# Kernel optimization log

Hardware: AMD Instinct MI355X
Metric: run time of the kernel (lower is better)

The kernel has to match this reference:

```python
import jax, jax.numpy as jnp
import numpy as np

N, P = 25000, 400000          # atoms, pairs
F, E, EH = 64, 32, 64         # nr_atom_basis, nr_edge_basis, nr_edge_basis_hidden
FH, SSH, S = 64, 64, 64       # node hidden, spatial hidden, spatial
FV, C, H, K = 64, 32, 4, 50   # velocity hidden, coefficients, heads, rbf
R_MAX = 0.5                   # maximum_interaction_radius (nm)
EPS = 1e-8
SCALE = 1.0                   # scale_factor_in_nanometer


def physnet_rbf(d):
    # PhysNet RBF: exp(-beta * (exp(-d) - mu_k)^2), mu_k in [exp(-r_max), 1]
    mu = jnp.linspace(np.exp(-R_MAX), 1.0, K).astype(jnp.float32)
    beta = jnp.float32(((2.0 / K) * (1.0 - np.exp(-R_MAX))) ** -2)
    return jnp.exp(-beta * (jnp.exp(-d)[:, None] - mu) ** 2)  # [P, K]


def seg_sum(v, idx, n):
    return jax.ops.segment_sum(v, idx, num_segments=n)


def seg_mean(v, idx, n):
    # matches torch scatter_reduce 'mean' with include_self=False (empty segments -> 0)
    s = seg_sum(v, idx, n)
    cnt = seg_sum(jnp.ones((v.shape[0],), v.dtype), idx, n)
    cnt = jnp.maximum(cnt, 1.0).reshape((n,) + (1,) * (v.ndim - 1))
    return s / cnt


def seg_softmax(a, idx, n):
    # numerically-stable per-receiver softmax over variable neighbor sets
    m = jax.ops.segment_max(a, idx, num_segments=n)
    m = jnp.where(jnp.isfinite(m), m, 0.0)
    e = jnp.exp(a - m[idx])
    return e / seg_sum(e, idx, n)[idx]


def setup_inputs():
    key = jax.random.key(0)
    ks = jax.random.split(key, 20)
    def w(k, shape):
        return jax.random.normal(k, shape, jnp.float32) * 0.05
    z = lambda *s: jnp.zeros(s, jnp.float32)
    return dict(
        h=jax.random.normal(ks[0], (N, F), jnp.float32),
        x=jax.random.uniform(ks[1], (N, 3), jnp.float32),
        v=jax.random.normal(ks[2], (N, 3), jnp.float32) * 0.1,
        idx_i=jax.random.randint(ks[3], (P,), 0, N),
        idx_j=jax.random.randint(ks[4], (P,), 0, N),
        W_ein=w(ks[5], (2 * F, K)), b_ein=z(K),
        W_eo1=w(ks[6], (2 * F + K + 1, EH)), b_eo1=z(EH),
        W_eo2=w(ks[7], (EH, E)), b_eo2=z(E),
        W_att=w(ks[8], (E, H)), b_att=z(H),
        W_xm=w(ks[9], (H * E, C)),
        W_vm=w(ks[10], (C,)),
        W_pn1=w(ks[11], (C, SSH)), b_pn1=z(SSH),
        W_pn2=w(ks[12], (SSH, S)), b_pn2=z(S),
        W_n1=w(ks[13], (F + H * E + S, FH)), b_n1=z(FH),
        W_n2=w(ks[14], (FH, F)), b_n2=z(F),
        W_v1=w(ks[15], (F, FV)), b_v1=z(FV),
        W_v2=w(ks[16], (FV, 1)),
    )


def reference(h, x, v, idx_i, idx_j,
              W_ein, b_ein, W_eo1, b_eo1, W_eo2, b_eo2,
              W_att, b_att, W_xm, W_vm,
              W_pn1, b_pn1, W_pn2, b_pn2,
              W_n1, b_n1, W_n2, b_n2,
              W_v1, b_v1, W_v2):
    act = jax.nn.silu
    # geometry
    r_ij = x[idx_j] - x[idx_i]                       # [P, 3]
    d_ij = jnp.sqrt(jnp.sum(r_ij ** 2, axis=-1) + EPS)
    dir_ij = r_ij / (d_ij[:, None] + EPS)
    # edge update (Eq. 7): RBF-filtered edge MLP
    h_cat = jnp.concatenate([h[idx_i], h[idx_j]], axis=-1)          # [P, 2F]
    filtered = physnet_rbf(d_ij) * (h_cat @ W_ein + b_ein)          # [P, K]
    edge_in = jnp.concatenate([h_cat, filtered, (d_ij / SCALE)[:, None]], axis=-1)
    h_ij_edge = act(edge_in @ W_eo1 + b_eo1) @ W_eo2 + b_eo2        # [P, E]
    # multi-head semantic attention: segment softmax per receiver
    att = jax.nn.celu(h_ij_edge @ W_att + b_att, alpha=2.0)         # [P, H]
    att_w = seg_softmax(att, idx_i, N)                              # [P, H]
    h_ij_sem = (h_ij_edge[:, :, None] * att_w[:, None, :]).reshape(P, E * H)
    # neighborhood aggregation
    h_i_sem = seg_sum(h_ij_sem, idx_i, N)                           # [N, E*H]
    # spatial attention (Eq. 6)
    comb = jnp.tanh(h_ij_sem @ W_xm)[:, :, None] * dir_ij[:, None, :]  # [P, C, 3]
    comb_mean = seg_mean(comb, idx_i, N)                            # [N, C, 3]
    comb_norm2 = jnp.sum(comb_mean ** 2, axis=-1)                   # [N, C]
    h_i_spatial = act(act(comb_norm2 @ W_pn1 + b_pn1) @ W_pn2 + b_pn2)
    # node update (Eq. 4)
    node_in = jnp.concatenate([h, h_i_sem, h_i_spatial], axis=-1)
    h_new = h + act(act(node_in @ W_n1 + b_n1) @ W_n2 + b_n2)
    # velocity update (Eq. 12)
    v_ij = jnp.einsum('pcx,c->px', comb, W_vm)                      # [P, 3]
    dv = seg_mean(v_ij, idx_i, N)                                   # [N, 3]
    gate = 2.0 * jax.nn.sigmoid(act(h_new @ W_v1 + b_v1) @ W_v2)    # [N, 1]
    v_new = gate * v + dv
    x_new = x + v_new
    return h_new, x_new, v_new
```

## Files before the change

kernel.cpp:

```cpp
#include <hip/hip_runtime.h>
#include <hip/hip_bf16.h>

#define DEV __device__ __forceinline__

constexpr int N_ = 25000;
constexpr int P_ = 400000;

constexpr int align4(int xx){ return (xx+3)&~3; }
constexpr int OFF_CNT     = 0;
constexpr int OFF_OFFSETS = align4(OFF_CNT + N_);
constexpr int OFF_CURSOR  = align4(OFF_OFFSETS + N_ + 1);
constexpr int OFF_EDGE    = align4(OFF_CURSOR + N_);
constexpr int OFF_E4      = OFF_EDGE + P_*16;
constexpr int OFF_DIR     = OFF_E4 + P_*4;
constexpr int OFF_SEM     = align4(OFF_DIR + P_*4);
constexpr int OFF_N2      = OFF_SEM + N_*64;
constexpr int OFF_DV      = OFF_N2 + N_*16;
constexpr int OFF_WB5     = OFF_DV + N_*4;
constexpr int OFF_WB6     = OFF_WB5 + 1024;
constexpr int OFF_WB7     = OFF_WB6 + 2048;
constexpr int OFF_WB8     = OFF_WB7 + 8192;
constexpr int OFF_WB9     = OFF_WB8 + 2048;
constexpr int OFF_HB      = OFF_WB9 + 2048;
constexpr int OFF_SIJ     = OFF_HB + N_*32;
constexpr int OFF_WB1     = OFF_SIJ + P_*2;
constexpr int OFF_WB2     = OFF_WB1 + 8192;
constexpr int OFF_WB3     = OFF_WB2 + 2048;
constexpr int OFF_WB4     = OFF_WB3 + 1024;
constexpr int WS_UNITS    = OFF_WB4 + 2048;

constexpr float MU0F  = 0.60653065971263342f;
constexpr float DMUF  = (1.0f - 0.60653065971263342f) / 49.0f;
constexpr float BETAF = 1.0f / ((0.04f * (1.0f - 0.60653065971263342f)) *
                                (0.04f * (1.0f - 0.60653065971263342f)));
constexpr float EPSF  = 1e-8f;

DEV float u2f(unsigned int u){ union{unsigned int i; float f;} c; c.i=u; return c.f; }
DEV unsigned int f2b16(float f){
  __hip_bfloat16 b = __float2bfloat16(f);
  unsigned short s; __builtin_memcpy(&s, &b, 2);
  return (unsigned int)s;
}
DEV unsigned int pack2(float a, float b){ return f2b16(a) | (f2b16(b) << 16); }
DEV float frcp(float x){ return __builtin_amdgcn_rcpf(x); }
DEV float silu_f(float v){ return v * frcp(1.0f + __expf(-v)); }

using short8 = __attribute__((ext_vector_type(8))) short;
using f32x4  = __attribute__((ext_vector_type(4))) float;
union U4S8 { uint4 u; short8 s; };
DEV short8 ld_frag(const void* p){ U4S8 c; c.u = *(const uint4*)p; return c.s; }
DEV f32x4 mfma16(short8 a, short8 b, f32x4 c){
  return __builtin_amdgcn_mfma_f32_16x16x32_bf16(a, b, c, 0, 0, 0);
}

__global__ void k_prep0(const int* __restrict__ idx_i,
                        const float* __restrict__ h,
                        const float* __restrict__ Wein, const float* __restrict__ Weo1,
                        const float* __restrict__ Weo2, const float* __restrict__ Wxm,
                        const float* __restrict__ Wpn1, const float* __restrict__ Wpn2,
                        const float* __restrict__ Wn1,  const float* __restrict__ Wn2,
                        const float* __restrict__ Wv1,
                        int* __restrict__ cnt, unsigned int* __restrict__ hb,
                        unsigned short* __restrict__ wb1, unsigned short* __restrict__ wb2,
                        unsigned short* __restrict__ wb3, unsigned short* __restrict__ wb4,
                        unsigned short* __restrict__ wb5, unsigned short* __restrict__ wb6,
                        unsigned short* __restrict__ wb7, unsigned short* __restrict__ wb8,
                        unsigned short* __restrict__ wb9){
  int t = blockIdx.x*256 + threadIdx.x;
  const int st = gridDim.x*256;
  if (t < P_) atomicAdd(&cnt[idx_i[t]], 1);
  for (int q=t; q<N_*32; q+=st){
    float2 a = *(const float2*)(h + (size_t)q*2);
    hb[q] = pack2(a.x, a.y);
  }
  for (int q=t; q<8*4*64*8; q+=st){
    int e=q&7, lane=(q>>3)&63, sx=(q>>9)&3, nf=q>>11;
    int l15=lane&15, quad=lane>>4;
    int n = 16*nf + l15, k = sx*32 + quad*8 + e;
    float v = (n<50) ? Wein[k*50+n] : ((n<64) ? 0.f : Weo1[k*64+(n-64)]);
    wb1[q] = (unsigned short)f2b16(v);
  }
  for (int q=t; q<4*2*64*8; q+=st){
    int e=q&7, lane=(q>>3)&63, sx=(q>>9)&1, nf=q>>10;
    int l15=lane&15, quad=lane>>4;
    int n = 16*nf + l15, k = sx*32 + quad*8 + e;
    float v = (k<50) ? Weo1[(128+k)*64+n] : ((k==50) ? Weo1[178*64+n] : 0.f);
    wb2[q] = (unsigned short)f2b16(v);
  }
  for (int q=t; q<2*2*64*8; q+=st){
    int e=q&7, lane=(q>>3)&63, sx=(q>>9)&1, nf=q>>10;
    int l15=lane&15, quad=lane>>4;
    int n = 16*nf + l15, k = sx*32 + quad*8 + e;
    wb3[q] = (unsigned short)f2b16(Weo2[k*32+n]);
  }
  for (int q=t; q<8*64*8; q+=st){
    int e=q&7, lane=(q>>3)&63, nf=q>>9;
    int l15=lane&15, quad=lane>>4;
    int k = quad*8 + e;
    int n_log = l15*8 + nf;
    int cc = n_log>>2, hh = n_log&3;
    wb4[q] = (unsigned short)f2b16(Wxm[(k*4+hh)*32 + cc]);
  }
  for (int q=t; q<4*64*8; q+=st){
    int e=q&7, lane=(q>>3)&63, nf=q>>9;
    int l15=lane&15, quad=lane>>4;
    int n = 16*nf + l15, k = quad*8 + e;
    wb5[q] = (unsigned short)f2b16(Wpn1[k*64+n]);
  }
  for (int q=t; q<4*2*64*8; q+=st){
    int e=q&7, lane=(q>>3)&63, sx=(q>>9)&1, nf=q>>10;
    int l15=lane&15, quad=lane>>4;
    int n = 16*nf + l15, k = sx*32 + quad*8 + e;
    wb6[q] = (unsigned short)f2b16(Wpn2[k*64+n]);
    wb8[q] = (unsigned short)f2b16(Wn2[k*64+n]);
    wb9[q] = (unsigned short)f2b16(Wv1[k*64+n]);
  }
  for (int q=t; q<4*8*64*8; q+=st){
    int e=q&7, lane=(q>>3)&63, sx=(q>>9)&7, nf=q>>12;
    int l15=lane&15, quad=lane>>4;
    int n = 16*nf + l15, k = sx*32 + quad*8 + e;
    wb7[q] = (unsigned short)f2b16(Wn1[k*64+n]);
  }
}

__global__ __launch_bounds__(1024) void k_scan(const int* __restrict__ cnt,
                                               int* __restrict__ offsets,
                                               int* __restrict__ cursor){
  __shared__ unsigned short sCnt[N_];
  __shared__ int swv[16];
  const int t = threadIdx.x;
  const int wv = t >> 6, ln = t & 63;
  for (int q = t; q < N_; q += 1024) sCnt[q] = (unsigned short)cnt[q];
  __syncthreads();
  constexpr int CH = (N_ + 1023)/1024;
  int b = t*CH, e = b+CH;
  if (b > N_) b = N_;
  if (e > N_) e = N_;
  int s = 0;
  for (int q=b; q<e; q++) s += sCnt[q];
  int incl = s;
  #pragma unroll
  for (int off=1; off<64; off<<=1){
    int vv = __shfl_up(incl, off);
    if (ln >= off) incl += vv;
  }
  if (ln == 63) swv[wv] = incl;
  __syncthreads();
  if (wv == 0 && ln < 16){
    int w = swv[ln];
    #pragma unroll
    for (int off=1; off<16; off<<=1){
      int vv = __shfl_up(w, off);
      if (ln >= off) w += vv;
    }
    swv[ln] = w;
  }
  __syncthreads();
  const int wpre = (wv > 0) ? swv[wv-1] : 0;
  int run = wpre + incl - s;
  for (int q=b; q<e; q++){
    int c0 = sCnt[q];
    offsets[q] = run; cursor[q] = run; run += c0;
  }
  if (t == 1023) offsets[N_] = run;
}

__global__ void k_scatter2(const int* __restrict__ idx_i, const int* __restrict__ idx_j,
                           int* __restrict__ cursor,
                           int* __restrict__ sij){
  int t = blockIdx.x*256 + threadIdx.x;
  if (t >= P_) return;
  int i = idx_i[t], j = idx_j[t];
  int pos = atomicAdd(&cursor[i], 1);
  *(int2*)(sij + (size_t)pos*2) = make_int2(i, j);
}

__global__ __launch_bounds__(256, 4) void k_edge2(
    const unsigned short* __restrict__ hb,
    const int* __restrict__ sij, const float* __restrict__ x,
    float* __restrict__ dir4,
    const unsigned short* __restrict__ wb1, const unsigned short* __restrict__ wb2,
    const unsigned short* __restrict__ wb3,
    const float* __restrict__ bein, const float* __restrict__ beo1,
    const float* __restrict__ beo2, const float* __restrict__ Watt,
    const float* __restrict__ batt,
    unsigned int* __restrict__ edge_out, float* __restrict__ e4_out)
{
  __shared__ __align__(16) unsigned char sAll[4*4608];
  __shared__ float sdv[128];
  __shared__ float semd[128];

  const int tid  = threadIdx.x;
  const int wv   = tid >> 6;
  const int lane = tid & 63;
  const int l15  = lane & 15;
  const int quad = lane >> 4;
  const int pbase = blockIdx.x * 128;
  unsigned char* sW = sAll + wv*4608;

  if (lane < 32){
    int row = 32*wv + lane;
    int2 ij = *(const int2*)(sij + (size_t)(pbase + row)*2);
    float xi0=x[ij.x*3], xi1=x[ij.x*3+1], xi2=x[ij.x*3+2];
    float xj0=x[ij.y*3], xj1=x[ij.y*3+1], xj2=x[ij.y*3+2];
    float rx=xj0-xi0, ry=xj1-xi1, rz=xj2-xi2;
    float d = sqrtf(rx*rx+ry*ry+rz*rz+EPSF);
    float iv = frcp(d+EPSF);
    sdv[row]  = d;
    semd[row] = __expf(-d);
    *(float4*)(dir4 + (size_t)(pbase + row)*4) = make_float4(rx*iv, ry*iv, rz*iv, d);
  }

  short8 af0[4], af1[4];
  {
    const int rbase = pbase + 32*wv;
    int2 ij0 = *(const int2*)(sij + (size_t)(rbase + l15)*2);
    int2 ij1 = *(const int2*)(sij + (size_t)(rbase + 16 + l15)*2);
    const unsigned char* hB = (const unsigned char*)hb;
    af0[0] = ld_frag(hB + (size_t)ij0.x*128 + quad*16);
    af0[1] = ld_frag(hB + (size_t)ij0.x*128 + 64 + quad*16);
    af0[2] = ld_frag(hB + (size_t)ij0.y*128 + quad*16);
    af0[3] = ld_frag(hB + (size_t)ij0.y*128 + 64 + quad*16);
    af1[0] = ld_frag(hB + (size_t)ij1.x*128 + quad*16);
    af1[1] = ld_frag(hB + (size_t)ij1.x*128 + 64 + quad*16);
    af1[2] = ld_frag(hB + (size_t)ij1.y*128 + quad*16);
    af1[3] = ld_frag(hB + (size_t)ij1.y*128 + 64 + quad*16);
  }

  f32x4 acc[2][4];
  #pragma unroll
  for (int mf=0; mf<2; mf++)
    #pragma unroll
    for (int nf=0; nf<4; nf++){
      int nn = 16*nf + l15;
      float bias = (nn < 50) ? bein[nn] : 0.f;
      acc[mf][nf] = (f32x4){bias, bias, bias, bias};
    }
  #pragma unroll
  for (int s=0; s<4; s++){
    #pragma unroll
    for (int nf=0; nf<4; nf++){
      short8 b = ld_frag((const unsigned char*)wb1 + (size_t)((nf*4 + s)*64 + lane)*16);
      acc[0][nf] = mfma16(af0[s], b, acc[0][nf]);
      acc[1][nf] = mfma16(af1[s], b, acc[1][nf]);
    }
  }

  #pragma unroll
  for (int mf=0; mf<2; mf++)
    #pragma unroll
    for (int nf=0; nf<4; nf++){
      int n = 16*nf + l15;
      float mu = MU0F + (float)n*DMUF;
      #pragma unroll
      for (int reg=0; reg<4; reg++){
        int lrow = 16*mf + quad*4 + reg;
        int grow = 32*wv + lrow;
        float t = semd[grow] - mu;
        float fv = acc[mf][nf][reg] * __expf(-BETAF*t*t);
        unsigned short ob;
        if (n < 50)       ob = (unsigned short)f2b16(fv);
        else if (n == 50) ob = (unsigned short)f2b16(sdv[grow]);
        else              ob = 0;
        ((unsigned short*)sW)[lrow*72 + n] = ob;
      }
    }

  #pragma unroll
  for (int mf=0; mf<2; mf++)
    #pragma unroll
    for (int nf=0; nf<4; nf++){
      float bias = beo1[16*nf + l15];
      acc[mf][nf] = (f32x4){bias, bias, bias, bias};
    }
  #pragma unroll
  for (int s=0; s<4; s++){
    #pragma unroll
    for (int nf=0; nf<4; nf++){
      short8 b = ld_frag((const unsigned char*)wb1 + (size_t)(((4+nf)*4 + s)*64 + lane)*16);
      acc[0][nf] = mfma16(af0[s], b, acc[0][nf]);
      acc[1][nf] = mfma16(af1[s], b, acc[1][nf]);
    }
  }

  #pragma unroll
  for (int s=0; s<2; s++){
    int koff = s*32 + quad*8;
    short8 a0 = ld_frag(sW + l15*144      + koff*2);
    short8 a1 = ld_frag(sW + (16+l15)*144 + koff*2);
    #pragma unroll
    for (int nf=0; nf<4; nf++){
      short8 b = ld_frag((const unsigned char*)wb2 + (size_t)((nf*2 + s)*64 + lane)*16);
      acc[0][nf] = mfma16(a0, b, acc[0][nf]);
      acc[1][nf] = mfma16(a1, b, acc[1][nf]);
    }
  }

  unsigned char* A3 = sW;
  #pragma unroll
  for (int mf=0; mf<2; mf++)
    #pragma unroll
    for (int nf=0; nf<4; nf++){
      int n = 16*nf + l15;
      #pragma unroll
      for (int reg=0; reg<4; reg++){
        int lrow = 16*mf + quad*4 + reg;
        ((unsigned short*)A3)[lrow*72 + n] = (unsigned short)f2b16(silu_f(acc[mf][nf][reg]));
      }
    }

  f32x4 acc3[2][2];
  #pragma unroll
  for (int mf=0; mf<2; mf++)
    #pragma unroll
    for (int nf=0; nf<2; nf++){
      float bias = beo2[16*nf + l15];
      acc3[mf][nf] = (f32x4){bias, bias, bias, bias};
    }
  #pragma unroll
  for (int s=0; s<2; s++){
    int koff = s*32 + quad*8;
    short8 a0 = ld_frag(A3 + l15*144      + koff*2);
    short8 a1 = ld_frag(A3 + (16+l15)*144 + koff*2);
    #pragma unroll
    for (int nf=0; nf<2; nf++){
      short8 b = ld_frag((const unsigned char*)wb3 + (size_t)((nf*2 + s)*64 + lane)*16);
      acc3[0][nf] = mfma16(a0, b, acc3[0][nf]);
      acc3[1][nf] = mfma16(a1, b, acc3[1][nf]);
    }
  }

  #pragma unroll
  for (int mf=0; mf<2; mf++)
    #pragma unroll
    for (int nf=0; nf<2; nf++){
      int n = 16*nf + l15;
      #pragma unroll
      for (int reg=0; reg<4; reg++){
        int lrow = 16*mf + quad*4 + reg;
        ((float*)sW)[lrow*36 + n] = acc3[mf][nf][reg];
      }
    }

  {
    int rr = lane >> 1;
    int p = pbase + 32*wv + rr;
    int cb = (lane & 1) * 16;
    const float* er = (const float*)(sW + rr*144);
    float l0, l1, l2, l3;
    if ((lane & 1) == 0){ l0 = batt[0]; l1 = batt[1]; l2 = batt[2]; l3 = batt[3]; }
    else                { l0 = l1 = l2 = l3 = 0.f; }
    float ecache[16];
    {
      float4 v0 = *(const float4*)(er + cb);
      float4 v1 = *(const float4*)(er + cb + 4);
      float4 v2 = *(const float4*)(er + cb + 8);
      float4 v3 = *(const float4*)(er + cb + 12);
      ecache[0]=v0.x; ecache[1]=v0.y; ecache[2]=v0.z; ecache[3]=v0.w;
      ecache[4]=v1.x; ecache[5]=v1.y; ecache[6]=v1.z; ecache[7]=v1.w;
      ecache[8]=v2.x; ecache[9]=v2.y; ecache[10]=v2.z; ecache[11]=v2.w;
      ecache[12]=v3.x; ecache[13]=v3.y; ecache[14]=v3.z; ecache[15]=v3.w;
    }
    #pragma unroll
    for (int c=0;c<16;c++){
      float ev = ecache[c];
      const float4 wr = *(const float4*)(Watt + (cb + c)*4);
      l0 += ev*wr.x; l1 += ev*wr.y; l2 += ev*wr.z; l3 += ev*wr.w;
    }
    l0 += __shfl_xor(l0,1); l1 += __shfl_xor(l1,1);
    l2 += __shfl_xor(l2,1); l3 += __shfl_xor(l3,1);
    if ((lane & 1) == 0){
      float e0 = __expf(l0 > 0.f ? l0 : 2.f*(__expf(l0*0.5f)-1.f));
      float e1 = __expf(l1 > 0.f ? l1 : 2.f*(__expf(l1*0.5f)-1.f));
      float e2 = __expf(l2 > 0.f ? l2 : 2.f*(__expf(l2*0.5f)-1.f));
      float e3 = __expf(l3 > 0.f ? l3 : 2.f*(__expf(l3*0.5f)-1.f));
      *(float4*)(e4_out + (size_t)p*4) = make_float4(e0, e1, e2, e3);
    }
    uint4 o1 = make_uint4(pack2(ecache[0],ecache[1]),  pack2(ecache[2],ecache[3]),
                          pack2(ecache[4],ecache[5]),  pack2(ecache[6],ecache[7]));
    uint4 o2 = make_uint4(pack2(ecache[8],ecache[9]),  pack2(ecache[10],ecache[11]),
                          pack2(ecache[12],ecache[13]),pack2(ecache[14],ecache[15]));
    unsigned int* ep = edge_out + (size_t)p*16 + (lane&1)*8;
    *(uint4*)(ep)     = o1;
    *(uint4*)(ep + 4) = o2;
  }
}

__global__ __launch_bounds__(256, 4) void k_agg(
    const int* __restrict__ offsets,
    const unsigned int* __restrict__ edgeb,
    const float* __restrict__ e4,
    const float* __restrict__ dir4,
    const unsigned short* __restrict__ wb4,
    const float* __restrict__ Wvm,
    unsigned int* __restrict__ semB, unsigned int* __restrict__ n2B,
    float* __restrict__ wsDv)
{
  __shared__ __align__(16) unsigned char sAllB[4*5632];
  const int wv   = threadIdx.x >> 6;
  const int lane = threadIdx.x & 63;
  unsigned char* sA = sAllB + wv*5632;
  unsigned char* gC = sA + 1024;
  float* sE = (float*)(sA + 5120);
  float* sD = (float*)(sA + 5376);

  const int c    = lane & 31;
  const int l15  = lane & 15;
  const int quad = lane >> 4;
  const int half = lane >> 5;
  const bool low = (lane < 32);

  short8 b4[8];
  #pragma unroll
  for (int nf=0; nf<8; nf++)
    b4[nf] = ld_frag((const unsigned char*)wb4 + (size_t)(nf*64 + lane)*16);
  const float wvm_c = Wvm[c];

  const int i = blockIdx.x*4 + wv;
  if (i >= N_) return;
  const int n0 = offsets[i], n1 = offsets[i+1];
  const int cnt = n1 - n0;

  {
    const int nc0 = min(16, cnt);
    if (lane < 32){
      if (lane*32 < nc0*64){
        const uint4* src = (const uint4*)(edgeb + (size_t)n0*16 + lane*8);
        *(uint4*)(sA + lane*32)      = src[0];
        *(uint4*)(sA + lane*32 + 16) = src[1];
      }
    } else if (lane < 48){
      int k = lane - 32;
      if (k < nc0) *(float4*)(sE + k*4) = *(const float4*)(e4 + (size_t)(n0+k)*4);
    } else {
      int k = lane - 48;
      if (k < nc0) *(float4*)(sD + k*4) = *(const float4*)(dir4 + (size_t)(n0+k)*4);
    }
  }

  float d0=0.f,d1=0.f,d2=0.f,d3=0.f;
  for (int s = n0 + lane; s < n1; s += 64){
    const float4 ev = *(const float4*)(e4 + (size_t)s*4);
    d0+=ev.x; d1+=ev.y; d2+=ev.z; d3+=ev.w;
  }
  #pragma unroll
  for (int off=32; off>=1; off>>=1){
    d0 += __shfl_xor(d0,off); d1 += __shfl_xor(d1,off);
    d2 += __shfl_xor(d2,off); d3 += __shfl_xor(d3,off);
  }
  const float i0 = (cnt>0)?frcp(d0):0.f, i1 = (cnt>0)?frcp(d1):0.f;
  const float i2 = (cnt>0)?frcp(d2):0.f, i3 = (cnt>0)?frcp(d3):0.f;

  float sem4[4] = {0.f,0.f,0.f,0.f};
  float cx=0.f,cy=0.f,cz=0.f, gx=0.f,gy=0.f,gz=0.f;

  bool staged = true;
  for (int base = n0; base < n1; base += 16){
    const int nc = min(16, n1 - base);
    if (!staged){
      if (lane < 32){
        if (lane*32 < nc*64){
          const uint4* src = (const uint4*)(edgeb + (size_t)base*16 + lane*8);
          *(uint4*)(sA + lane*32)      = src[0];
          *(uint4*)(sA + lane*32 + 16) = src[1];
        }
      } else if (lane < 48){
        int k = lane - 32;
        if (k < nc) *(float4*)(sE + k*4) = *(const float4*)(e4 + (size_t)(base+k)*4);
      } else {
        int k = lane - 48;
        if (k < nc) *(float4*)(sD + k*4) = *(const float4*)(dir4 + (size_t)(base+k)*4);
      }
    }
    staged = false;
    {
      short8 a0 = ld_frag(sA + l15*64 + quad*16);
      f32x4 accg[8];
      #pragma unroll
      for (int nf=0; nf<8; nf++){
        f32x4 z = (f32x4){0.f,0.f,0.f,0.f};
        accg[nf] = mfma16(a0, b4[nf], z);
      }
      #pragma unroll
      for (int reg=0; reg<4; reg++){
        int row = quad*4 + reg;
        uint4 o = make_uint4(pack2(accg[0][reg],accg[1][reg]),
                             pack2(accg[2][reg],accg[3][reg]),
                             pack2(accg[4][reg],accg[5][reg]),
                             pack2(accg[6][reg],accg[7][reg]));
        *(uint4*)(gC + row*256 + l15*16) = o;
      }
    }
    for (int t0 = 0; t0 < nc; t0 += 2){
      const int rloc = t0 + half;
      const bool act = rloc < nc;
      const int rc = act ? rloc : 0;
      const float4 ev = *(const float4*)(sE + rc*4);
      const float4 dv = *(const float4*)(sD + rc*4);
      const float aw0 = ev.x*i0, aw1 = ev.y*i1, aw2 = ev.z*i2, aw3 = ev.w*i3;
      uint2 gv = *(const uint2*)(gC + rc*256 + c*8);
      float g0=u2f(gv.x<<16), g1=u2f(gv.x&0xffff0000u);
      float g2=u2f(gv.y<<16), g3=u2f(gv.y&0xffff0000u);
      float tp = aw0*g0 + aw1*g1 + aw2*g2 + aw3*g3;
      float tt = fminf(fmaxf(tp, -15.f), 15.f);
      float ex = __expf(2.f*tt);
      float th = (ex-1.f)*frcp(ex+1.f);
      unsigned int ew = *(const unsigned int*)(sA + rc*64 + (c>>1)*4);
      float ec = (c & 1) ? u2f(ew & 0xffff0000u) : u2f(ew << 16);
      if (act){
        sem4[0] += ec*aw0; sem4[1] += ec*aw1;
        sem4[2] += ec*aw2; sem4[3] += ec*aw3;
        cx += th*dv.x; cy += th*dv.y; cz += th*dv.z;
        float tw = th*wvm_c;
        gx += tw*dv.x; gy += tw*dv.y; gz += tw*dv.z;
      }
    }
  }

  #pragma unroll
  for (int j=0;j<4;j++) sem4[j] += __shfl_xor(sem4[j], 32);
  cx += __shfl_xor(cx,32); cy += __shfl_xor(cy,32); cz += __shfl_xor(cz,32);
  #pragma unroll
  for (int off=32; off>=1; off>>=1){
    gx += __shfl_xor(gx,off); gy += __shfl_xor(gy,off); gz += __shfl_xor(gz,off);
  }
  const float invc = frcp((float)(cnt > 1 ? cnt : 1));
  if (low){
    float mx = cx*invc, my = cy*invc, mz = cz*invc;
    float n2v = mx*mx + my*my + mz*mz;
    float n2o = __shfl_xor(n2v, 1);
    if ((c & 1) == 0) n2B[(size_t)i*16 + (c>>1)] = pack2(n2v, n2o);
    *(uint2*)(semB + (size_t)i*64 + c*2) =
        make_uint2(pack2(sem4[0],sem4[1]), pack2(sem4[2],sem4[3]));
  }
  if (lane == 0)
    *(float4*)(wsDv + (size_t)i*4) = make_float4(gx*invc, gy*invc, gz*invc, 0.f);
}

__global__ __launch_bounds__(64) void k_mlp(
    const float* __restrict__ h, const float* __restrict__ x, const float* __restrict__ v,
    const unsigned short* __restrict__ hb,
    const unsigned short* __restrict__ semB, const unsigned short* __restrict__ n2B,
    const float* __restrict__ wsDv,
    const unsigned short* __restrict__ wb5, const unsigned short* __restrict__ wb6,
    const unsigned short* __restrict__ wb7, const unsigned short* __restrict__ wb8,
    const unsigned short* __restrict__ wb9,
    const float* __restrict__ bpn1, const float* __restrict__ bpn2,
    const float* __restrict__ bn1,  const float* __restrict__ bn2,
    const float* __restrict__ bv1,  const float* __restrict__ Wv2,
    float* __restrict__ out)
{
  __shared__ __align__(16) unsigned char sT[16*136];
  __shared__ __align__(16) unsigned char sU[16*136];

  const int lane = threadIdx.x & 63;
  const int l15  = lane & 15;
  const int quad = lane >> 4;
  const int base = blockIdx.x*16;
  const int r0a  = min(base + l15, N_-1);
  const unsigned char* hB  = (const unsigned char*)hb;
  const unsigned char* sB  = (const unsigned char*)semB;
  const unsigned char* nB  = (const unsigned char*)n2B;

  {
    f32x4 acc[4];
    #pragma unroll
    for (int nf=0; nf<4; nf++){ float b = bpn1[16*nf+l15]; acc[nf] = (f32x4){b,b,b,b}; }
    short8 a0 = ld_frag(nB + (size_t)r0a*64 + quad*16);
    #pragma unroll
    for (int nf=0; nf<4; nf++){
      short8 b = ld_frag((const unsigned char*)wb5 + (size_t)(nf*64 + lane)*16);
      acc[nf] = mfma16(a0, b, acc[nf]);
    }
    #pragma unroll
    for (int nf=0; nf<4; nf++){
      int n = 16*nf + l15;
      #pragma unroll
      for (int reg=0; reg<4; reg++){
        int row = quad*4 + reg;
        ((unsigned short*)(sT + row*136))[n] = (unsigned short)f2b16(silu_f(acc[nf][reg]));
      }
    }
  }
  {
    f32x4 acc[4];
    #pragma unroll
    for (int nf=0; nf<4; nf++){ float b = bpn2[16*nf+l15]; acc[nf] = (f32x4){b,b,b,b}; }
    #pragma unroll
    for (int s=0; s<2; s++){
      int koff = s*32 + quad*8;
      short8 a0 = ld_frag(sT + l15*136 + koff*2);
      #pragma unroll
      for (int nf=0; nf<4; nf++){
        short8 b = ld_frag((const unsigned char*)wb6 + (size_t)((nf*2 + s)*64 + lane)*16);
        acc[nf] = mfma16(a0, b, acc[nf]);
      }
    }
    #pragma unroll
    for (int nf=0; nf<4; nf++){
      int n = 16*nf + l15;
      #pragma unroll
      for (int reg=0; reg<4; reg++){
        int row = quad*4 + reg;
        ((unsigned short*)(sU + row*136))[n] = (unsigned short)f2b16(silu_f(acc[nf][reg]));
      }
    }
  }
  {
    f32x4 acc[4];
    #pragma unroll
    for (int nf=0; nf<4; nf++){ float b = bn1[16*nf+l15]; acc[nf] = (f32x4){b,b,b,b}; }
    #pragma unroll
    for (int s=0; s<8; s++){
      int koff = s*32 + quad*8;
      short8 a0;
      if (koff < 64){
        a0 = ld_frag(hB + (size_t)r0a*128 + koff*2);
      } else if (koff < 192){
        a0 = ld_frag(sB + (size_t)r0a*256 + (koff-64)*2);
      } else {
        a0 = ld_frag(sU + l15*136 + (koff-192)*2);
      }
      #pragma unroll
      for (int nf=0; nf<4; nf++){
        short8 b = ld_frag((const unsigned char*)wb7 + (size_t)((nf*8 + s)*64 + lane)*16);
        acc[nf] = mfma16(a0, b, acc[nf]);
      }
    }
    #pragma unroll
    for (int nf=0; nf<4; nf++){
      int n = 16*nf + l15;
      #pragma unroll
      for (int reg=0; reg<4; reg++){
        int row = quad*4 + reg;
        ((unsigned short*)(sT + row*136))[n] = (unsigned short)f2b16(silu_f(acc[nf][reg]));
      }
    }
  }
  {
    f32x4 acc[4];
    #pragma unroll
    for (int nf=0; nf<4; nf++){ float b = bn2[16*nf+l15]; acc[nf] = (f32x4){b,b,b,b}; }
    #pragma unroll
    for (int s=0; s<2; s++){
      int koff = s*32 + quad*8;
      short8 a0 = ld_frag(sT + l15*136 + koff*2);
      #pragma unroll
      for (int nf=0; nf<4; nf++){
        short8 b = ld_frag((const unsigned char*)wb8 + (size_t)((nf*2 + s)*64 + lane)*16);
        acc[nf] = mfma16(a0, b, acc[nf]);
      }
    }
    #pragma unroll
    for (int nf=0; nf<4; nf++){
      int n = 16*nf + l15;
      #pragma unroll
      for (int reg=0; reg<4; reg++){
        int row = quad*4 + reg;
        int node = base + row;
        float hv = (node < N_) ? h[(size_t)node*64 + n] : 0.f;
        float hnew = hv + silu_f(acc[nf][reg]);
        if (node < N_) out[(size_t)node*64 + n] = hnew;
        ((unsigned short*)(sU + row*136))[n] = (unsigned short)f2b16(hnew);
      }
    }
  }
  {
    f32x4 acc[4];
    #pragma unroll
    for (int nf=0; nf<4; nf++){ float b = bv1[16*nf+l15]; acc[nf] = (f32x4){b,b,b,b}; }
    #pragma unroll
    for (int s=0; s<2; s++){
      int koff = s*32 + quad*8;
      short8 a0 = ld_frag(sU + l15*136 + koff*2);
      #pragma unroll
      for (int nf=0; nf<4; nf++){
        short8 b = ld_frag((const unsigned char*)wb9 + (size_t)((nf*2 + s)*64 + lane)*16);
        acc[nf] = mfma16(a0, b, acc[nf]);
      }
    }
    float part[4] = {0.f,0.f,0.f,0.f};
    #pragma unroll
    for (int nf=0; nf<4; nf++){
      float w2 = Wv2[16*nf + l15];
      #pragma unroll
      for (int reg=0; reg<4; reg++)
        part[reg] += silu_f(acc[nf][reg]) * w2;
    }
    #pragma unroll
    for (int reg=0; reg<4; reg++){
      #pragma unroll
      for (int off=1; off<16; off<<=1)
        part[reg] += __shfl_xor(part[reg], off);
    }
    if (l15 == 0){
      #pragma unroll
      for (int reg=0; reg<4; reg++){
        int row = quad*4 + reg;
        int node = base + row;
        if (node < N_){
          float gate = 2.f*frcp(1.f + __expf(-part[reg]));
          float4 dvv = *(const float4*)(wsDv + (size_t)node*4);
          float dvs[3] = {dvv.x, dvv.y, dvv.z};
          #pragma unroll
          for (int ax=0; ax<3; ax++){
            float vn = gate * v[(size_t)node*3 + ax] + dvs[ax];
            out[(size_t)N_*64 + (size_t)node*3 + ax]                 = x[(size_t)node*3 + ax] + vn;
            out[(size_t)N_*64 + (size_t)N_*3 + (size_t)node*3 + ax]  = vn;
          }
        }
      }
    }
  }
}

extern "C" void kernel_launch(void* const* d_in, const int* in_sizes, int n_in,
                              void* d_out, int out_size, void* d_ws, size_t ws_size,
                              hipStream_t stream)
{
  const float* h = (const float*)d_in[0];
  const float* x = (const float*)d_in[1];
  const float* v = (const float*)d_in[2];
  const int* idx_i = (const int*)d_in[3];
  const int* idx_j = (const int*)d_in[4];
  const float* Wein = (const float*)d_in[5];  const float* bein = (const float*)d_in[6];
  const float* Weo1 = (const float*)d_in[7];  const float* beo1 = (const float*)d_in[8];
  const float* Weo2 = (const float*)d_in[9];  const float* beo2 = (const float*)d_in[10];
  const float* Watt = (const float*)d_in[11]; const float* batt = (const float*)d_in[12];
  const float* Wxm  = (const float*)d_in[13]; const float* Wvm  = (const float*)d_in[14];
  const float* Wpn1 = (const float*)d_in[15]; const float* bpn1 = (const float*)d_in[16];
  const float* Wpn2 = (const float*)d_in[17]; const float* bpn2 = (const float*)d_in[18];
  const float* Wn1  = (const float*)d_in[19]; const float* bn1  = (const float*)d_in[20];
  const float* Wn2  = (const float*)d_in[21]; const float* bn2  = (const float*)d_in[22];
  const float* Wv1  = (const float*)d_in[23]; const float* bv1  = (const float*)d_in[24];
  const float* Wv2  = (const float*)d_in[25];

  float* wsf        = (float*)d_ws;
  int*   cnt        = (int*)(wsf + OFF_CNT);
  int*   offsets    = (int*)(wsf + OFF_OFFSETS);
  int*   cursor     = (int*)(wsf + OFF_CURSOR);
  unsigned int* edgeb = (unsigned int*)(wsf + OFF_EDGE);
  float* e4o        = wsf + OFF_E4;
  float* diro       = wsf + OFF_DIR;
  unsigned int* semB = (unsigned int*)(wsf + OFF_SEM);
  unsigned int* n2B  = (unsigned int*)(wsf + OFF_N2);
  float* wsDv       = wsf + OFF_DV;
  unsigned short* wb1 = (unsigned short*)(wsf + OFF_WB1);
  unsigned short* wb2 = (unsigned short*)(wsf + OFF_WB2);
  unsigned short* wb3 = (unsigned short*)(wsf + OFF_WB3);
  unsigned short* wb4 = (unsigned short*)(wsf + OFF_WB4);
  unsigned short* wb5 = (unsigned short*)(wsf + OFF_WB5);
  unsigned short* wb6 = (unsigned short*)(wsf + OFF_WB6);
  unsigned short* wb7 = (unsigned short*)(wsf + OFF_WB7);
  unsigned short* wb8 = (unsigned short*)(wsf + OFF_WB8);
  unsigned short* wb9 = (unsigned short*)(wsf + OFF_WB9);
  unsigned int*   hb  = (unsigned int*)(wsf + OFF_HB);
  int*            sij = (int*)(wsf + OFF_SIJ);

  hipMemsetAsync(cnt, 0, N_*sizeof(int), stream);
  k_prep0<<<(P_+255)/256, 256, 0, stream>>>(idx_i, h, Wein, Weo1, Weo2, Wxm,
                                            Wpn1, Wpn2, Wn1, Wn2, Wv1,
                                            cnt, hb, wb1, wb2, wb3, wb4,
                                            wb5, wb6, wb7, wb8, wb9);
  k_scan<<<1, 1024, 0, stream>>>(cnt, offsets, cursor);
  k_scatter2<<<(P_+255)/256, 256, 0, stream>>>(idx_i, idx_j, cursor, sij);
  k_edge2<<<P_/128, 256, 0, stream>>>((const unsigned short*)hb, sij, x, diro,
                                      wb1, wb2, wb3,
                                      bein, beo1, beo2, Watt, batt,
                                      edgeb, e4o);
  k_agg<<<(N_+3)/4, 256, 0, stream>>>(offsets, edgeb, e4o, diro, wb4, Wvm,
                                      semB, n2B, wsDv);
  k_mlp<<<(N_+15)/16, 64, 0, stream>>>(h, x, v,
                                       (const unsigned short*)hb,
                                       (const unsigned short*)semB,
                                       (const unsigned short*)n2B,
                                       wsDv,
                                       wb5, wb6, wb7, wb8, wb9,
                                       bpn1, bpn2, bn1, bn2, bv1, Wv2,
                                       (float*)d_out);
}
```

Baseline: 299.7 us.

## Record histogram ranks to drop scatter atomics and overlap scan with prep

The histogram kernel now saves each edge's atomicAdd return value as its rank within its receiver bucket. The scatter then computes each edge's position as offset plus rank, with no second round of atomics on a cursor array. The h/weight bf16 conversion moves out of the histogram kernel into the single-block scan launch, running on 64 extra blocks beside the scan block. The cost is an extra P-sized rank array written and read through global memory.

```diff
diff --git a/kernel.cpp b/kernel.cpp
--- a/kernel.cpp
+++ b/kernel.cpp
@@ -27,7 +27,8 @@
 constexpr int OFF_WB2     = OFF_WB1 + 8192;
 constexpr int OFF_WB3     = OFF_WB2 + 2048;
 constexpr int OFF_WB4     = OFF_WB3 + 1024;
-constexpr int WS_UNITS    = OFF_WB4 + 2048;
+constexpr int OFF_RANK    = OFF_WB4 + 2048;
+constexpr int WS_UNITS    = OFF_RANK + P_;
 
 constexpr float MU0F  = 0.60653065971263342f;
 constexpr float DMUF  = (1.0f - 0.60653065971263342f) / 49.0f;
@@ -53,22 +54,65 @@
   return __builtin_amdgcn_mfma_f32_16x16x32_bf16(a, b, c, 0, 0, 0);
 }
 
-__global__ void k_prep0(const int* __restrict__ idx_i,
-                        const float* __restrict__ h,
-                        const float* __restrict__ Wein, const float* __restrict__ Weo1,
-                        const float* __restrict__ Weo2, const float* __restrict__ Wxm,
-                        const float* __restrict__ Wpn1, const float* __restrict__ Wpn2,
-                        const float* __restrict__ Wn1,  const float* __restrict__ Wn2,
-                        const float* __restrict__ Wv1,
-                        int* __restrict__ cnt, unsigned int* __restrict__ hb,
-                        unsigned short* __restrict__ wb1, unsigned short* __restrict__ wb2,
-                        unsigned short* __restrict__ wb3, unsigned short* __restrict__ wb4,
-                        unsigned short* __restrict__ wb5, unsigned short* __restrict__ wb6,
-                        unsigned short* __restrict__ wb7, unsigned short* __restrict__ wb8,
-                        unsigned short* __restrict__ wb9){
+__global__ void k_hist(const int* __restrict__ idx_i,
+                       int* __restrict__ cnt, int* __restrict__ rank){
   int t = blockIdx.x*256 + threadIdx.x;
-  const int st = gridDim.x*256;
-  if (t < P_) atomicAdd(&cnt[idx_i[t]], 1);
+  if (t < P_) rank[t] = atomicAdd(&cnt[idx_i[t]], 1);
+}
+
+__global__ __launch_bounds__(1024) void k_scan2(
+    const int* __restrict__ cnt, int* __restrict__ offsets,
+    const float* __restrict__ h,
+    const float* __restrict__ Wein, const float* __restrict__ Weo1,
+    const float* __restrict__ Weo2, const float* __restrict__ Wxm,
+    const float* __restrict__ Wpn1, const float* __restrict__ Wpn2,
+    const float* __restrict__ Wn1,  const float* __restrict__ Wn2,
+    const float* __restrict__ Wv1,
+    unsigned int* __restrict__ hb,
+    unsigned short* __restrict__ wb1, unsigned short* __restrict__ wb2,
+    unsigned short* __restrict__ wb3, unsigned short* __restrict__ wb4,
+    unsigned short* __restrict__ wb5, unsigned short* __restrict__ wb6,
+    unsigned short* __restrict__ wb7, unsigned short* __restrict__ wb8,
+    unsigned short* __restrict__ wb9){
+  __shared__ unsigned short sCnt[N_];
+  __shared__ int swv[16];
+  if (blockIdx.x == 0){
+    const int t = threadIdx.x;
+    const int wv = t >> 6, ln = t & 63;
+    for (int q = t; q < N_; q += 1024) sCnt[q] = (unsigned short)cnt[q];
+    __syncthreads();
+    constexpr int CH = (N_ + 1023)/1024;
+    int b = t*CH, e = b+CH;
+    if (b > N_) b = N_;
+    if (e > N_) e = N_;
+    int s = 0;
+    for (int q=b; q<e; q++) s += sCnt[q];
+    int incl = s;
+    #pragma unroll
+    for (int off=1; off<64; off<<=1){
+      int vv = __shfl_up(incl, off);
+      if (ln >= off) incl += vv;
+    }
+    if (ln == 63) swv[wv] = incl;
+    __syncthreads();
+    if (wv == 0 && ln < 16){
+      int w = swv[ln];
+      #pragma unroll
+      for (int off=1; off<16; off<<=1){
+        int vv = __shfl_up(w, off);
+        if (ln >= off) w += vv;
+      }
+      swv[ln] = w;
+    }
+    __syncthreads();
+    const int wpre = (wv > 0) ? swv[wv-1] : 0;
+    int run = wpre + incl - s;
+    for (int q=b; q<e; q++){ offsets[q] = run; run += sCnt[q]; }
+    if (t == 1023) offsets[N_] = run;
+    return;
+  }
+  int t = (blockIdx.x-1)*1024 + threadIdx.x;
+  const int st = (gridDim.x-1)*1024;
   for (int q=t; q<N_*32; q+=st){
     float2 a = *(const float2*)(h + (size_t)q*2);
     hb[q] = pack2(a.x, a.y);
@@ -123,55 +167,13 @@
   }
 }
 
-__global__ __launch_bounds__(1024) void k_scan(const int* __restrict__ cnt,
-                                               int* __restrict__ offsets,
-                                               int* __restrict__ cursor){
-  __shared__ unsigned short sCnt[N_];
-  __shared__ int swv[16];
-  const int t = threadIdx.x;
-  const int wv = t >> 6, ln = t & 63;
-  for (int q = t; q < N_; q += 1024) sCnt[q] = (unsigned short)cnt[q];
-  __syncthreads();
-  constexpr int CH = (N_ + 1023)/1024;
-  int b = t*CH, e = b+CH;
-  if (b > N_) b = N_;
-  if (e > N_) e = N_;
-  int s = 0;
-  for (int q=b; q<e; q++) s += sCnt[q];
-  int incl = s;
-  #pragma unroll
-  for (int off=1; off<64; off<<=1){
-    int vv = __shfl_up(incl, off);
-    if (ln >= off) incl += vv;
-  }
-  if (ln == 63) swv[wv] = incl;
-  __syncthreads();
-  if (wv == 0 && ln < 16){
-    int w = swv[ln];
-    #pragma unroll
-    for (int off=1; off<16; off<<=1){
-      int vv = __shfl_up(w, off);
-      if (ln >= off) w += vv;
-    }
-    swv[ln] = w;
-  }
-  __syncthreads();
-  const int wpre = (wv > 0) ? swv[wv-1] : 0;
-  int run = wpre + incl - s;
-  for (int q=b; q<e; q++){
-    int c0 = sCnt[q];
-    offsets[q] = run; cursor[q] = run; run += c0;
-  }
-  if (t == 1023) offsets[N_] = run;
-}
-
-__global__ void k_scatter2(const int* __restrict__ idx_i, const int* __restrict__ idx_j,
-                           int* __restrict__ cursor,
+__global__ void k_scatter3(const int* __restrict__ idx_i, const int* __restrict__ idx_j,
+                           const int* __restrict__ offsets, const int* __restrict__ rank,
                            int* __restrict__ sij){
   int t = blockIdx.x*256 + threadIdx.x;
   if (t >= P_) return;
   int i = idx_i[t], j = idx_j[t];
-  int pos = atomicAdd(&cursor[i], 1);
+  int pos = offsets[i] + rank[t];
   *(int2*)(sij + (size_t)pos*2) = make_int2(i, j);
 }
 
@@ -738,7 +740,6 @@
   float* wsf        = (float*)d_ws;
   int*   cnt        = (int*)(wsf + OFF_CNT);
   int*   offsets    = (int*)(wsf + OFF_OFFSETS);
-  int*   cursor     = (int*)(wsf + OFF_CURSOR);
   unsigned int* edgeb = (unsigned int*)(wsf + OFF_EDGE);
   float* e4o        = wsf + OFF_E4;
   float* diro       = wsf + OFF_DIR;
@@ -756,14 +757,16 @@
   unsigned short* wb9 = (unsigned short*)(wsf + OFF_WB9);
   unsigned int*   hb  = (unsigned int*)(wsf + OFF_HB);
   int*            sij = (int*)(wsf + OFF_SIJ);
+  int*            rnk = (int*)(wsf + OFF_RANK);
 
   hipMemsetAsync(cnt, 0, N_*sizeof(int), stream);
-  k_prep0<<<(P_+255)/256, 256, 0, stream>>>(idx_i, h, Wein, Weo1, Weo2, Wxm,
-                                            Wpn1, Wpn2, Wn1, Wn2, Wv1,
-                                            cnt, hb, wb1, wb2, wb3, wb4,
-                                            wb5, wb6, wb7, wb8, wb9);
-  k_scan<<<1, 1024, 0, stream>>>(cnt, offsets, cursor);
-  k_scatter2<<<(P_+255)/256, 256, 0, stream>>>(idx_i, idx_j, cursor, sij);
+  k_hist<<<(P_+255)/256, 256, 0, stream>>>(idx_i, cnt, rnk);
+  k_scan2<<<65, 1024, 0, stream>>>(cnt, offsets, h,
+                                   Wein, Weo1, Weo2, Wxm, Wpn1, Wpn2,
+                                   Wn1, Wn2, Wv1,
+                                   hb, wb1, wb2, wb3, wb4,
+                                   wb5, wb6, wb7, wb8, wb9);
+  k_scatter3<<<(P_+255)/256, 256, 0, stream>>>(idx_i, idx_j, offsets, rnk, sij);
   k_edge2<<<P_/128, 256, 0, stream>>>((const unsigned short*)hb, sij, x, diro,
                                       wb1, wb2, wb3,
                                       bein, beo1, beo2, Watt, batt,
```

After: 268.3 us. -10.5%, faster.
